# Kernel optimization log

Measured on AMD Instinct MI355X. Metric: run time of the kernel, lower is better.

The kernel has to match this reference:

```python
import jax, jax.numpy as jnp
import numpy as np

B, H, S, DK, DV = 2, 16, 2048, 64, 64


def setup_inputs() -> dict:
    key = jax.random.key(0)
    kq, kk, kv = jax.random.split(key, 3)
    queries = jax.random.normal(kq, (B, H, S, DK), dtype=jnp.float32)
    keys = jax.random.normal(kk, (B, H, S, DK), dtype=jnp.float32)
    values = jax.random.normal(kv, (B, H, S, DV), dtype=jnp.float32)
    # causal boolean mask, broadcastable over batch and heads
    mask = jnp.tril(jnp.ones((S, S), dtype=bool))[None, None, :, :]
    return {"queries": queries, "keys": keys, "values": values, "d_k": DK, "mask": mask}


def reference(queries, keys, values, d_k, mask):
    scale = 1.0 / jnp.sqrt(jnp.float32(d_k))
    # scores: [B, H, S, S]
    scores = jnp.einsum("bhqd,bhkd->bhqk", queries, keys) * scale
    mask_f = mask.astype(jnp.float32)
    scores = scores + (-1e9) * (1.0 - mask_f)
    weights = jax.nn.softmax(scores, axis=-1)
    # second mask step from the original: min(|mask|, |weights|)
    weights = jnp.minimum(jnp.abs(mask_f), jnp.abs(weights))
    return jnp.einsum("bhqk,bhkd->bhqd", weights, values)
```

## Files before the change

kernel.cpp:

```cpp
#include <hip/hip_runtime.h>
#include <hip/hip_bf16.h>

#define B_ 2
#define H_ 16
#define S_ 2048
#define D_ 64

typedef __attribute__((ext_vector_type(8))) short bf16x8;
typedef __attribute__((ext_vector_type(8))) unsigned short u16x8;
typedef __attribute__((ext_vector_type(4))) unsigned int u32x4;
typedef __attribute__((ext_vector_type(4))) float f32x4;
typedef unsigned short ushort_t;

#define SCALE 0.18033688011112042f

__device__ __forceinline__ unsigned short f2bf(float x) {
  unsigned int u = __builtin_bit_cast(unsigned int, x);
  unsigned int r = (u + 0x7FFFu + ((u >> 16) & 1u)) >> 16;
  return (unsigned short)r;
}

__device__ __forceinline__ unsigned int cvt_pk_bf16(float lo, float hi) {
  unsigned int r;
  asm("v_cvt_pk_bf16_f32 %0, %1, %2" : "=v"(r) : "v"(lo), "v"(hi));
  return r;
}

__device__ __forceinline__ float fast_exp2(float x) {
  float r;
  asm("v_exp_f32 %0, %1" : "=v"(r) : "v"(x));
  return r;
}

__device__ __forceinline__ float fmax3(float a, float b, float c) {
  return fmaxf(fmaxf(a, b), c);
}

__device__ __forceinline__ int sigma32(int lr) {
  return (lr & 3) | ((lr & 0x0C) << 1) | ((lr & 0x10) >> 2);
}

#define GLL16(gp, lp)                                                          \
  __builtin_amdgcn_global_load_lds(                                            \
      (const __attribute__((address_space(1))) unsigned int*)(gp),             \
      (__attribute__((address_space(3))) unsigned int*)(lp), 16, 0, 0)

__global__ void prepack32(const float* __restrict__ Kf, const float* __restrict__ Vf,
                          ushort_t* __restrict__ Kg, ushort_t* __restrict__ Vtg) {
  const int blk = blockIdx.x;
  const int tid = threadIdx.x;
  const int bh = blk >> 6, kt = blk & 63;
  const float* srcK = Kf + ((size_t)bh * S_ + (size_t)kt * 32) * D_;
  const float* srcV = Vf + ((size_t)bh * S_ + (size_t)kt * 32) * D_;
  ushort_t* dK = Kg + (size_t)blk * 2048;
  ushort_t* dV = Vtg + (size_t)blk * 2048;
  const int e = tid * 8;
  {
    const int lr = e >> 6, pos = (e >> 3) & 7, ch = pos ^ (lr & 7);
    const float* sp = srcK + sigma32(lr) * 64 + ch * 8;
    float4 a = *(const float4*)sp;
    float4 b = *(const float4*)(sp + 4);
    u16x8 w;
    w[0] = f2bf(a.x); w[1] = f2bf(a.y); w[2] = f2bf(a.z); w[3] = f2bf(a.w);
    w[4] = f2bf(b.x); w[5] = f2bf(b.y); w[6] = f2bf(b.z); w[7] = f2bf(b.w);
    *(u16x8*)(dK + e) = w;
  }
  {
    const int d0 = e >> 5, pos2 = (e >> 3) & 3, ch2 = pos2 ^ (d0 & 3);
    u16x8 w;
    for (int i = 0; i < 8; ++i) w[i] = f2bf(srcV[(size_t)(ch2 * 8 + i) * 64 + d0]);
    *(u16x8*)(dV + e) = w;
  }
}

__launch_bounds__(256, 8)
__global__ void attn_s32(const float* __restrict__ Qf, const ushort_t* __restrict__ Kg,
                         const ushort_t* __restrict__ Vtg, float* __restrict__ O,
                         float* __restrict__ PO, float* __restrict__ ML) {
  const int bh = blockIdx.x;
  const int y = blockIdx.y;
  int qt, c;
  if (y == 0) { qt = 15; c = 0; }
  else if (y <= 16) { qt = 15 + y; c = 0; }
  else if (y == 17) { qt = 31; c = 1; }
  else { const int p = y - 18, k = 15 - (p >> 1);
         if (p & 1) { qt = k + 15; c = 1; } else { qt = k - 1; c = 0; } }
  const int t0k = c << 5;
  const int tEnd = 2 * qt + 1;
  const int t1k = (tEnd < t0k + 31) ? tEnd : (t0k + 31);

  const int tid = threadIdx.x;
  const int wave = tid >> 6, lane = tid & 63;
  const int col = lane & 15, g = lane >> 4;

  __shared__ __align__(16) ushort_t Kl[2][32][64];
  __shared__ __align__(16) ushort_t Vt[2][64][32];

  const int qrow = qt * 64 + wave * 16 + col;
  bf16x8 qf[2];
  {
    const float* Qh = Qf + (size_t)bh * S_ * D_;
    for (int kk = 0; kk < 2; ++kk) {
      const float* p = Qh + (size_t)qrow * 64 + kk * 32 + g * 8;
      float4 a = *(const float4*)p;
      float4 b = *(const float4*)(p + 4);
      float v[8] = {a.x, a.y, a.z, a.w, b.x, b.y, b.z, b.w};
      bf16x8 w;
      for (int i = 0; i < 8; ++i) w[i] = (short)f2bf(v[i] * SCALE);
      qf[kk] = w;
    }
  }

  f32x4 acc[4] = {};
  float m_ = -INFINITY, l_ = 0.0f;

  const int ch0 = (g ^ (col & 7)) << 3;
  const int ch1 = ((4 | g) ^ (col & 7)) << 3;
  const int chV = (g ^ (col & 3)) << 3;

  auto STAGE = [&](int kt, int b) {
    const ushort_t* kg = Kg + ((size_t)(bh * 64 + kt)) * 2048;
    const ushort_t* vg = Vtg + ((size_t)(bh * 64 + kt)) * 2048;
    GLL16(kg + tid * 8, &Kl[b][0][0] + tid * 8);
    GLL16(vg + tid * 8, &Vt[b][0][0] + tid * 8);
  };

  auto COMPUTE = [&](int kt, int b, bool diag) {
    f32x4 s[2] = {{0,0,0,0},{0,0,0,0}};
    __builtin_amdgcn_s_setprio(1);
    #pragma unroll
    for (int nt = 0; nt < 2; ++nt) {
      const ushort_t* row = &Kl[b][nt * 16 + col][0];
      const bf16x8 kf0 = *(const bf16x8*)(row + ch0);
      const bf16x8 kf1 = *(const bf16x8*)(row + ch1);
      s[nt] = __builtin_amdgcn_mfma_f32_16x16x32_bf16(kf0, qf[0], s[nt], 0, 0, 0);
      s[nt] = __builtin_amdgcn_mfma_f32_16x16x32_bf16(kf1, qf[1], s[nt], 0, 0, 0);
    }
    __builtin_amdgcn_s_setprio(0);
    if (diag) {
      const int qg = qt * 64 + wave * 16 + col - 32 * kt - 8 * g;
      #pragma unroll
      for (int nt = 0; nt < 2; ++nt)
        #pragma unroll
        for (int r = 0; r < 4; ++r)
          if (4 * nt + r > qg) s[nt][r] = -INFINITY;
    }
    float pm = fmax3(fmax3(s[0][0], s[0][1], s[0][2]),
                     fmax3(s[0][3], s[1][0], s[1][1]),
                     fmaxf(fmaxf(s[1][2], s[1][3]), -INFINITY));
    pm = fmaxf(pm, __shfl_xor(pm, 16));
    pm = fmaxf(pm, __shfl_xor(pm, 32));
    float fac = 1.0f;
    if (!__all(pm - m_ <= 8.0f)) {
      const float mn = fmaxf(m_, pm);
      fac = fast_exp2(m_ - mn);
      m_ = mn;
      #pragma unroll
      for (int nt = 0; nt < 4; ++nt) acc[nt] *= fac;
    }
    #pragma unroll
    for (int nt = 0; nt < 2; ++nt)
      #pragma unroll
      for (int r = 0; r < 4; ++r) s[nt][r] = fast_exp2(s[nt][r] - m_);
    const float b0 = (s[0][0] + s[0][1]) + (s[0][2] + s[0][3]);
    const float b1 = (s[1][0] + s[1][1]) + (s[1][2] + s[1][3]);
    l_ = l_ * fac + (b0 + b1);
    u32x4 w;
    w[0] = cvt_pk_bf16(s[0][0], s[0][1]); w[1] = cvt_pk_bf16(s[0][2], s[0][3]);
    w[2] = cvt_pk_bf16(s[1][0], s[1][1]); w[3] = cvt_pk_bf16(s[1][2], s[1][3]);
    const bf16x8 pf = __builtin_bit_cast(bf16x8, w);
    __builtin_amdgcn_s_setprio(1);
    #pragma unroll
    for (int nt = 0; nt < 4; ++nt) {
      const bf16x8 vf = *(const bf16x8*)(&Vt[b][nt * 16 + col][0] + chV);
      acc[nt] = __builtin_amdgcn_mfma_f32_16x16x32_bf16(vf, pf, acc[nt], 0, 0, 0);
    }
    __builtin_amdgcn_s_setprio(0);
  };

  int cur = 0;
  STAGE(t0k, 0);
  __syncthreads();
  const int diag0 = 2 * qt;
  for (int kt = t0k; kt <= t1k; ++kt) {
    if (kt < t1k) STAGE(kt + 1, cur ^ 1);
    COMPUTE(kt, cur, kt >= diag0);
    __syncthreads();
    cur ^= 1;
  }

  float lsum = l_;
  lsum += __shfl_xor(lsum, 16);
  lsum += __shfl_xor(lsum, 32);
  const int rowloc = wave * 16 + col;
  if (qt <= 15) {
    const float inv = 1.0f / lsum;
    float* dst = O + (size_t)bh * S_ * D_ + (size_t)qrow * 64;
    #pragma unroll
    for (int nt = 0; nt < 4; ++nt) {
      f32x4 v = acc[nt];
      v *= inv;
      *(f32x4*)(dst + nt * 16 + 4 * g) = v;
    }
  } else {
    float* po = PO + (size_t)((((bh << 4) + (qt - 16)) << 1) + c) * 4096;
    #pragma unroll
    for (int nt = 0; nt < 4; ++nt)
      *(f32x4*)(po + rowloc * 64 + nt * 16 + 4 * g) = acc[nt];
    if (g == 0) {
      float* ml = ML + (size_t)((((bh << 4) + (qt - 16)) << 1) + c) * 128 + rowloc * 2;
      ml[0] = m_;
      ml[1] = lsum;
    }
  }
}

__global__ void merge_partials(const float* __restrict__ PO, const float* __restrict__ ML,
                               float* __restrict__ O) {
  const int bh = blockIdx.x;
  const int q16 = blockIdx.y;
  const int tid = threadIdx.x;
  const int r = tid >> 2, d0 = (tid & 3) << 4;
  const size_t base = (size_t)((bh << 4) + q16) << 1;
  const float* ml0 = ML + base * 128 + r * 2;
  const float* ml1 = ML + (base + 1) * 128 + r * 2;
  const float m0 = ml0[0], l0 = ml0[1], m1 = ml1[0], l1 = ml1[1];
  const float M = fmaxf(m0, m1);
  const float w0 = fast_exp2(m0 - M), w1 = fast_exp2(m1 - M);
  const float inv = 1.0f / (w0 * l0 + w1 * l1);
  const float a = w0 * inv, b = w1 * inv;
  const float* p0 = PO + base * 4096 + r * 64 + d0;
  const float* p1 = PO + (base + 1) * 4096 + r * 64 + d0;
  float* out = O + ((size_t)bh * S_ + (size_t)(16 + q16) * 64 + r) * 64 + d0;
  #pragma unroll
  for (int j = 0; j < 4; ++j) {
    float4 x = *(const float4*)(p0 + 4 * j);
    float4 y = *(const float4*)(p1 + 4 * j);
    float4 o;
    o.x = a * x.x + b * y.x; o.y = a * x.y + b * y.y;
    o.z = a * x.z + b * y.z; o.w = a * x.w + b * y.w;
    *(float4*)(out + 4 * j) = o;
  }
}

__device__ __forceinline__ int sigma_row64(int rl) {
  return (rl & 0x23) | ((rl & 0x0C) << 1) | ((rl & 0x10) >> 2);
}
__launch_bounds__(256, 4)
__global__ void attn_fb(const float* __restrict__ Qf, const float* __restrict__ Kf,
                        const float* __restrict__ Vf, float* __restrict__ O) {
  const int bh = blockIdx.x;
  const int qt = 31 - blockIdx.y;
  const int tid = threadIdx.x;
  const int wave = tid >> 6, lane = tid & 63;
  const int col = lane & 15, g = lane >> 4;
  __shared__ __align__(16) ushort_t Kl[2][64][64];
  __shared__ __align__(16) ushort_t Vt[2][64][64];
  const int qrow = qt * 64 + wave * 16 + col;
  bf16x8 qf[2];
  {
    const float* Qh = Qf + (size_t)bh * S_ * D_;
    for (int kk = 0; kk < 2; ++kk) {
      const float* p = Qh + (size_t)qrow * 64 + kk * 32 + g * 8;
      float4 a = *(const float4*)p;
      float4 b = *(const float4*)(p + 4);
      float v[8] = {a.x, a.y, a.z, a.w, b.x, b.y, b.z, b.w};
      bf16x8 w;
      for (int i = 0; i < 8; ++i) w[i] = (short)f2bf(v[i] * SCALE);
      qf[kk] = w;
    }
  }
  f32x4 acc[4] = {};
  float m_ = -INFINITY, l_ = 0.0f;
  const int ch0 = (g ^ (col & 7)) << 3;
  const int ch1 = ((4 | g) ^ (col & 7)) << 3;
  auto STAGE = [&](int t, int b) {
    const float* Kh = Kf + (size_t)bh * S_ * D_;
    const float* Vh = Vf + (size_t)bh * S_ * D_;
    {
      const int rl = tid >> 2;
      const int c0 = (tid & 3) << 4;
      const float* src = Kh + ((size_t)(t * 64 + sigma_row64(rl))) * 64 + c0;
      for (int jj = 0; jj < 2; ++jj) {
        float4 x = *(const float4*)(src + jj * 8);
        float4 y = *(const float4*)(src + jj * 8 + 4);
        u16x8 w;
        w[0] = f2bf(x.x); w[1] = f2bf(x.y); w[2] = f2bf(x.z); w[3] = f2bf(x.w);
        w[4] = f2bf(y.x); w[5] = f2bf(y.y); w[6] = f2bf(y.z); w[7] = f2bf(y.w);
        const int ch = (c0 >> 3) + jj;
        *(u16x8*)&Kl[b][rl][(ch ^ (rl & 7)) << 3] = w;
      }
    }
    {
      const int cc = tid & 63;
      const int r0 = (tid >> 6) << 4;
      const float* src = Vh + ((size_t)(t * 64 + r0)) * 64 + cc;
      for (int jj = 0; jj < 2; ++jj) {
        u16x8 w;
        for (int i = 0; i < 8; ++i) w[i] = f2bf(src[(size_t)(jj * 8 + i) * 64]);
        const int ch = (r0 >> 3) + jj;
        *(u16x8*)&Vt[b][cc][(ch ^ (cc & 7)) << 3] = w;
      }
    }
  };
  auto COMPUTE = [&](int b, bool diag) {
    f32x4 s[4] = {{0,0,0,0},{0,0,0,0},{0,0,0,0},{0,0,0,0}};
    for (int nt = 0; nt < 4; ++nt) {
      const ushort_t* row = &Kl[b][nt * 16 + col][0];
      const bf16x8 kf0 = *(const bf16x8*)(row + ch0);
      const bf16x8 kf1 = *(const bf16x8*)(row + ch1);
      s[nt] = __builtin_amdgcn_mfma_f32_16x16x32_bf16(kf0, qf[0], s[nt], 0, 0, 0);
      s[nt] = __builtin_amdgcn_mfma_f32_16x16x32_bf16(kf1, qf[1], s[nt], 0, 0, 0);
    }
    if (diag) {
      const int qloc = wave * 16 + col;
      for (int nt = 0; nt < 4; ++nt) {
        const int tb = 32 * (nt >> 1) + 4 * (nt & 1) + 8 * g;
        for (int r = 0; r < 4; ++r)
          if (tb + r > qloc) s[nt][r] = -INFINITY;
      }
    }
    float pm = -INFINITY;
    for (int nt = 0; nt < 4; ++nt)
      for (int r = 0; r < 4; ++r) pm = fmaxf(pm, s[nt][r]);
    pm = fmaxf(pm, __shfl_xor(pm, 16));
    pm = fmaxf(pm, __shfl_xor(pm, 32));
    float fac = 1.0f;
    if (!__all(pm - m_ <= 8.0f)) {
      const float mn = fmaxf(m_, pm);
      fac = fast_exp2(m_ - mn);
      m_ = mn;
      for (int nt = 0; nt < 4; ++nt) acc[nt] *= fac;
    }
    float sum = 0.0f;
    for (int nt = 0; nt < 4; ++nt)
      for (int r = 0; r < 4; ++r) {
        const float p = fast_exp2(s[nt][r] - m_);
        s[nt][r] = p;
        sum += p;
      }
    l_ = l_ * fac + sum;
    u32x4 t0, t1;
    t0[0] = cvt_pk_bf16(s[0][0], s[0][1]); t0[1] = cvt_pk_bf16(s[0][2], s[0][3]);
    t0[2] = cvt_pk_bf16(s[1][0], s[1][1]); t0[3] = cvt_pk_bf16(s[1][2], s[1][3]);
    t1[0] = cvt_pk_bf16(s[2][0], s[2][1]); t1[1] = cvt_pk_bf16(s[2][2], s[2][3]);
    t1[2] = cvt_pk_bf16(s[3][0], s[3][1]); t1[3] = cvt_pk_bf16(s[3][2], s[3][3]);
    const bf16x8 pf0 = __builtin_bit_cast(bf16x8, t0);
    const bf16x8 pf1 = __builtin_bit_cast(bf16x8, t1);
    for (int nt = 0; nt < 4; ++nt) {
      const ushort_t* row = &Vt[b][nt * 16 + col][0];
      const bf16x8 vf0 = *(const bf16x8*)(row + ch0);
      const bf16x8 vf1 = *(const bf16x8*)(row + ch1);
      acc[nt] = __builtin_amdgcn_mfma_f32_16x16x32_bf16(vf0, pf0, acc[nt], 0, 0, 0);
      acc[nt] = __builtin_amdgcn_mfma_f32_16x16x32_bf16(vf1, pf1, acc[nt], 0, 0, 0);
    }
  };
  int cur = 0;
  STAGE(0, 0);
  __syncthreads();
  for (int t = 0; t <= qt; ++t) {
    if (t < qt) STAGE(t + 1, cur ^ 1);
    COMPUTE(cur, t == qt);
    __syncthreads();
    cur ^= 1;
  }
  float lsum = l_;
  lsum += __shfl_xor(lsum, 16);
  lsum += __shfl_xor(lsum, 32);
  const float inv = 1.0f / lsum;
  float* dst = O + (size_t)bh * S_ * D_ + (size_t)qrow * 64;
  for (int nt = 0; nt < 4; ++nt) {
    f32x4 v = acc[nt];
    v *= inv;
    *(f32x4*)(dst + nt * 16 + 4 * g) = v;
  }
}

extern "C" void kernel_launch(void* const* d_in, const int* in_sizes, int n_in,
                              void* d_out, int out_size, void* d_ws, size_t ws_size,
                              hipStream_t stream) {
  const float* Q = (const float*)d_in[0];
  const float* K = (const float*)d_in[1];
  const float* V = (const float*)d_in[2];
  float* O = (float*)d_out;
  const size_t NE = (size_t)B_ * H_ * S_ * D_;
  const size_t needK = 2 * NE * sizeof(ushort_t);
  const size_t PO_elems = 32ull * 16 * 2 * 4096;
  const size_t ML_elems = 32ull * 16 * 2 * 128;
  const size_t needSplit = needK + (PO_elems + ML_elems) * sizeof(float);
  if (ws_size >= needSplit) {
    ushort_t* kg = (ushort_t*)d_ws;
    float* PO = (float*)((char*)d_ws + needK);
    float* ML = PO + PO_elems;
    prepack32<<<2048, 256, 0, stream>>>(K, V, kg, kg + NE);
    attn_s32<<<dim3(32, 48), 256, 0, stream>>>(Q, kg, kg + NE, O, PO, ML);
    merge_partials<<<dim3(32, 16), 256, 0, stream>>>(PO, ML, O);
  } else {
    attn_fb<<<dim3(32, 32), 256, 0, stream>>>(Q, K, V, O);
  }
}
```

Before: 54.83 us.

## Switch attention kernel to 32x32 MFMA with 64-key tiles and intra-block key split

The main attention kernel moves from 16x16x32 MFMA over 32-key tiles to 32x32x16 MFMA over 64-key tiles. Each pair of waves shares a 32-query block and splits each key tile in half, and the two partial softmax states are merged through LDS at the end. The prepack kernel now emits 64-row swizzled K and transposed V tiles, and the running max starts at a finite value. The aim is fewer loop iterations and barriers and better MFMA efficiency, at the cost of double the LDS per block, lower occupancy (launch bounds 4), and an extra cross-wave merge step.

```diff
diff --git a/kernel.cpp b/kernel.cpp
--- a/kernel.cpp
+++ b/kernel.cpp
@@ -9,6 +9,7 @@
 typedef __attribute__((ext_vector_type(8))) short bf16x8;
 typedef __attribute__((ext_vector_type(8))) unsigned short u16x8;
 typedef __attribute__((ext_vector_type(4))) unsigned int u32x4;
+typedef __attribute__((ext_vector_type(16))) float f32x16;
 typedef __attribute__((ext_vector_type(4))) float f32x4;
 typedef unsigned short ushort_t;
 
@@ -35,9 +36,24 @@
 __device__ __forceinline__ float fmax3(float a, float b, float c) {
   return fmaxf(fmaxf(a, b), c);
 }
-
-__device__ __forceinline__ int sigma32(int lr) {
-  return (lr & 3) | ((lr & 0x0C) << 1) | ((lr & 0x10) >> 2);
+__device__ __forceinline__ float vmax16(f32x16 v) {
+  float a = fmax3(v[0], v[1], v[2]);
+  float b = fmax3(v[3], v[4], v[5]);
+  float c = fmax3(v[6], v[7], v[8]);
+  float d = fmax3(v[9], v[10], v[11]);
+  float e = fmax3(v[12], v[13], v[14]);
+  return fmax3(fmax3(a, b, v[15]), fmax3(c, d, e), -INFINITY);
+}
+__device__ __forceinline__ float vsum16(f32x16 v) {
+  float a = (v[0] + v[1]) + (v[2] + v[3]);
+  float b = (v[4] + v[5]) + (v[6] + v[7]);
+  float c = (v[8] + v[9]) + (v[10] + v[11]);
+  float d = (v[12] + v[13]) + (v[14] + v[15]);
+  return (a + b) + (c + d);
+}
+
+__device__ __forceinline__ int sigma6(int rl) {
+  return (rl & 0x33) | ((rl & 4) << 1) | ((rl & 8) >> 1);
 }
 
 #define GLL16(gp, lp)                                                          \
@@ -45,110 +61,109 @@
       (const __attribute__((address_space(1))) unsigned int*)(gp),             \
       (__attribute__((address_space(3))) unsigned int*)(lp), 16, 0, 0)
 
-__global__ void prepack32(const float* __restrict__ Kf, const float* __restrict__ Vf,
-                          ushort_t* __restrict__ Kg, ushort_t* __restrict__ Vtg) {
+__global__ void prepack(const float* __restrict__ Kf, const float* __restrict__ Vf,
+                        ushort_t* __restrict__ Kg, ushort_t* __restrict__ Vtg) {
   const int blk = blockIdx.x;
   const int tid = threadIdx.x;
-  const int bh = blk >> 6, kt = blk & 63;
-  const float* srcK = Kf + ((size_t)bh * S_ + (size_t)kt * 32) * D_;
-  const float* srcV = Vf + ((size_t)bh * S_ + (size_t)kt * 32) * D_;
-  ushort_t* dK = Kg + (size_t)blk * 2048;
-  ushort_t* dV = Vtg + (size_t)blk * 2048;
-  const int e = tid * 8;
-  {
-    const int lr = e >> 6, pos = (e >> 3) & 7, ch = pos ^ (lr & 7);
-    const float* sp = srcK + sigma32(lr) * 64 + ch * 8;
-    float4 a = *(const float4*)sp;
-    float4 b = *(const float4*)(sp + 4);
-    u16x8 w;
-    w[0] = f2bf(a.x); w[1] = f2bf(a.y); w[2] = f2bf(a.z); w[3] = f2bf(a.w);
-    w[4] = f2bf(b.x); w[5] = f2bf(b.y); w[6] = f2bf(b.z); w[7] = f2bf(b.w);
-    *(u16x8*)(dK + e) = w;
-  }
-  {
-    const int d0 = e >> 5, pos2 = (e >> 3) & 3, ch2 = pos2 ^ (d0 & 3);
-    u16x8 w;
-    for (int i = 0; i < 8; ++i) w[i] = f2bf(srcV[(size_t)(ch2 * 8 + i) * 64 + d0]);
-    *(u16x8*)(dV + e) = w;
-  }
-}
-
-__launch_bounds__(256, 8)
-__global__ void attn_s32(const float* __restrict__ Qf, const ushort_t* __restrict__ Kg,
-                         const ushort_t* __restrict__ Vtg, float* __restrict__ O,
-                         float* __restrict__ PO, float* __restrict__ ML) {
+  const int bh = blk >> 5, j = blk & 31;
+  const float* srcK = Kf + ((size_t)bh * S_ + (size_t)j * 64) * D_;
+  const float* srcV = Vf + ((size_t)bh * S_ + (size_t)j * 64) * D_;
+  ushort_t* dK = Kg + (size_t)blk * 4096;
+  ushort_t* dV = Vtg + (size_t)blk * 4096;
+  for (int is = 0; is < 2; ++is) {
+    const int e = is * 2048 + tid * 8;
+    {
+      const int rl = e >> 6, pos = (e >> 3) & 7, ch = pos ^ (rl & 7);
+      const float* sp = srcK + sigma6(rl) * 64 + ch * 8;
+      float4 a = *(const float4*)sp;
+      float4 b = *(const float4*)(sp + 4);
+      u16x8 w;
+      w[0] = f2bf(a.x); w[1] = f2bf(a.y); w[2] = f2bf(a.z); w[3] = f2bf(a.w);
+      w[4] = f2bf(b.x); w[5] = f2bf(b.y); w[6] = f2bf(b.z); w[7] = f2bf(b.w);
+      *(u16x8*)(dK + e) = w;
+    }
+    {
+      const int d0 = e >> 6, pos = (e >> 3) & 7, ch = pos ^ (d0 & 7);
+      u16x8 w;
+      for (int i = 0; i < 8; ++i) w[i] = f2bf(srcV[(size_t)(ch * 8 + i) * 64 + d0]);
+      *(u16x8*)(dV + e) = w;
+    }
+  }
+}
+
+__launch_bounds__(256, 4)
+__global__ void attn_pp(const float* __restrict__ Qf, const ushort_t* __restrict__ Kg,
+                        const ushort_t* __restrict__ Vtg, float* __restrict__ O,
+                        float* __restrict__ PO, float* __restrict__ ML) {
   const int bh = blockIdx.x;
   const int y = blockIdx.y;
   int qt, c;
   if (y == 0) { qt = 15; c = 0; }
   else if (y <= 16) { qt = 15 + y; c = 0; }
   else if (y == 17) { qt = 31; c = 1; }
-  else { const int p = y - 18, k = 15 - (p >> 1);
-         if (p & 1) { qt = k + 15; c = 1; } else { qt = k - 1; c = 0; } }
-  const int t0k = c << 5;
-  const int tEnd = 2 * qt + 1;
-  const int t1k = (tEnd < t0k + 31) ? tEnd : (t0k + 31);
+  else { const int px = y - 18, k = 15 - (px >> 1);
+         if (px & 1) { qt = k + 15; c = 1; } else { qt = k - 1; c = 0; } }
+  const int j0 = c << 4;
+  const int j1 = (qt < j0 + 15) ? qt : (j0 + 15);
 
   const int tid = threadIdx.x;
   const int wave = tid >> 6, lane = tid & 63;
-  const int col = lane & 15, g = lane >> 4;
-
-  __shared__ __align__(16) ushort_t Kl[2][32][64];
-  __shared__ __align__(16) ushort_t Vt[2][64][32];
-
-  const int qrow = qt * 64 + wave * 16 + col;
-  bf16x8 qf[2];
+  const int qh = wave >> 1, p = wave & 1;
+  const int cq = lane & 31, hi = lane >> 5;
+
+  __shared__ __align__(16) ushort_t Kl[2][64][64];
+  __shared__ __align__(16) ushort_t Vt[2][64][64];
+  __shared__ float mlS[2][2][32][2];
+
+  const int qrow = qt * 64 + qh * 32 + cq;
+  bf16x8 qf[4];
   {
-    const float* Qh = Qf + (size_t)bh * S_ * D_;
-    for (int kk = 0; kk < 2; ++kk) {
-      const float* p = Qh + (size_t)qrow * 64 + kk * 32 + g * 8;
-      float4 a = *(const float4*)p;
-      float4 b = *(const float4*)(p + 4);
-      float v[8] = {a.x, a.y, a.z, a.w, b.x, b.y, b.z, b.w};
+    const float* qp = Qf + (size_t)bh * S_ * D_ + (size_t)qrow * D_ + 8 * hi;
+    #pragma unroll
+    for (int ks = 0; ks < 4; ++ks) {
+      float4 a = *(const float4*)(qp + ks * 16);
+      float4 b = *(const float4*)(qp + ks * 16 + 4);
       bf16x8 w;
-      for (int i = 0; i < 8; ++i) w[i] = (short)f2bf(v[i] * SCALE);
-      qf[kk] = w;
-    }
-  }
-
-  f32x4 acc[4] = {};
-  float m_ = -INFINITY, l_ = 0.0f;
-
-  const int ch0 = (g ^ (col & 7)) << 3;
-  const int ch1 = ((4 | g) ^ (col & 7)) << 3;
-  const int chV = (g ^ (col & 3)) << 3;
-
-  auto STAGE = [&](int kt, int b) {
-    const ushort_t* kg = Kg + ((size_t)(bh * 64 + kt)) * 2048;
-    const ushort_t* vg = Vtg + ((size_t)(bh * 64 + kt)) * 2048;
-    GLL16(kg + tid * 8, &Kl[b][0][0] + tid * 8);
-    GLL16(vg + tid * 8, &Vt[b][0][0] + tid * 8);
+      w[0] = (short)f2bf(a.x * SCALE); w[1] = (short)f2bf(a.y * SCALE);
+      w[2] = (short)f2bf(a.z * SCALE); w[3] = (short)f2bf(a.w * SCALE);
+      w[4] = (short)f2bf(b.x * SCALE); w[5] = (short)f2bf(b.y * SCALE);
+      w[6] = (short)f2bf(b.z * SCALE); w[7] = (short)f2bf(b.w * SCALE);
+      qf[ks] = w;
+    }
+  }
+
+  f32x16 acc0 = {}, acc1 = {};
+  float m_ = -30000.0f, l_ = 0.0f;
+  const int xk = cq & 7;
+
+  auto STAGE = [&](int j, int b) {
+    const ushort_t* kg = Kg + ((size_t)(bh * 32 + j)) * 4096;
+    const ushort_t* vg = Vtg + ((size_t)(bh * 32 + j)) * 4096;
+    GLL16(kg + tid * 8,        &Kl[b][0][0] + tid * 8);
+    GLL16(kg + 2048 + tid * 8, &Kl[b][0][0] + 2048 + tid * 8);
+    GLL16(vg + tid * 8,        &Vt[b][0][0] + tid * 8);
+    GLL16(vg + 2048 + tid * 8, &Vt[b][0][0] + 2048 + tid * 8);
   };
 
-  auto COMPUTE = [&](int kt, int b, bool diag) {
-    f32x4 s[2] = {{0,0,0,0},{0,0,0,0}};
+  auto COMPUTE = [&](int b, bool diag) {
+    f32x16 s = {};
+    const ushort_t* krow = &Kl[b][32 * p + cq][0];
     __builtin_amdgcn_s_setprio(1);
     #pragma unroll
-    for (int nt = 0; nt < 2; ++nt) {
-      const ushort_t* row = &Kl[b][nt * 16 + col][0];
-      const bf16x8 kf0 = *(const bf16x8*)(row + ch0);
-      const bf16x8 kf1 = *(const bf16x8*)(row + ch1);
-      s[nt] = __builtin_amdgcn_mfma_f32_16x16x32_bf16(kf0, qf[0], s[nt], 0, 0, 0);
-      s[nt] = __builtin_amdgcn_mfma_f32_16x16x32_bf16(kf1, qf[1], s[nt], 0, 0, 0);
+    for (int ks = 0; ks < 4; ++ks) {
+      const bf16x8 kf = *(const bf16x8*)(krow + (((2 * ks + hi) ^ xk) << 3));
+      s = __builtin_amdgcn_mfma_f32_32x32x16_bf16(kf, qf[ks], s, 0, 0, 0);
     }
     __builtin_amdgcn_s_setprio(0);
     if (diag) {
-      const int qg = qt * 64 + wave * 16 + col - 32 * kt - 8 * g;
+      const int lim = 32 * qh + cq - 32 * p;
       #pragma unroll
-      for (int nt = 0; nt < 2; ++nt)
-        #pragma unroll
-        for (int r = 0; r < 4; ++r)
-          if (4 * nt + r > qg) s[nt][r] = -INFINITY;
-    }
-    float pm = fmax3(fmax3(s[0][0], s[0][1], s[0][2]),
-                     fmax3(s[0][3], s[1][0], s[1][1]),
-                     fmaxf(fmaxf(s[1][2], s[1][3]), -INFINITY));
-    pm = fmaxf(pm, __shfl_xor(pm, 16));
+      for (int r = 0; r < 16; ++r) {
+        const int tau = 16 * (r >> 3) + 4 * ((r >> 2) & 1) + (r & 3) + 8 * hi;
+        if (tau > lim) s[r] = -INFINITY;
+      }
+    }
+    float pm = vmax16(s);
     pm = fmaxf(pm, __shfl_xor(pm, 32));
     float fac = 1.0f;
     if (!__all(pm - m_ <= 8.0f)) {
@@ -156,61 +171,103 @@
       fac = fast_exp2(m_ - mn);
       m_ = mn;
       #pragma unroll
-      for (int nt = 0; nt < 4; ++nt) acc[nt] *= fac;
+      for (int r = 0; r < 16; ++r) { acc0[r] *= fac; acc1[r] *= fac; }
     }
     #pragma unroll
-    for (int nt = 0; nt < 2; ++nt)
-      #pragma unroll
-      for (int r = 0; r < 4; ++r) s[nt][r] = fast_exp2(s[nt][r] - m_);
-    const float b0 = (s[0][0] + s[0][1]) + (s[0][2] + s[0][3]);
-    const float b1 = (s[1][0] + s[1][1]) + (s[1][2] + s[1][3]);
-    l_ = l_ * fac + (b0 + b1);
-    u32x4 w;
-    w[0] = cvt_pk_bf16(s[0][0], s[0][1]); w[1] = cvt_pk_bf16(s[0][2], s[0][3]);
-    w[2] = cvt_pk_bf16(s[1][0], s[1][1]); w[3] = cvt_pk_bf16(s[1][2], s[1][3]);
-    const bf16x8 pf = __builtin_bit_cast(bf16x8, w);
+    for (int r = 0; r < 16; ++r) s[r] = fast_exp2(s[r] - m_);
+    l_ = l_ * fac + vsum16(s);
+    u32x4 t0, t1;
+    t0[0] = cvt_pk_bf16(s[0], s[1]);   t0[1] = cvt_pk_bf16(s[2], s[3]);
+    t0[2] = cvt_pk_bf16(s[4], s[5]);   t0[3] = cvt_pk_bf16(s[6], s[7]);
+    t1[0] = cvt_pk_bf16(s[8], s[9]);   t1[1] = cvt_pk_bf16(s[10], s[11]);
+    t1[2] = cvt_pk_bf16(s[12], s[13]); t1[3] = cvt_pk_bf16(s[14], s[15]);
+    const bf16x8 pf0 = __builtin_bit_cast(bf16x8, t0);
+    const bf16x8 pf1 = __builtin_bit_cast(bf16x8, t1);
+    const ushort_t* v0 = &Vt[b][cq][0];
+    const ushort_t* v1 = &Vt[b][32 + cq][0];
     __builtin_amdgcn_s_setprio(1);
-    #pragma unroll
-    for (int nt = 0; nt < 4; ++nt) {
-      const bf16x8 vf = *(const bf16x8*)(&Vt[b][nt * 16 + col][0] + chV);
-      acc[nt] = __builtin_amdgcn_mfma_f32_16x16x32_bf16(vf, pf, acc[nt], 0, 0, 0);
+    {
+      const bf16x8 a00 = *(const bf16x8*)(v0 + (((4 * p + hi) ^ xk) << 3));
+      const bf16x8 a01 = *(const bf16x8*)(v0 + (((4 * p + 2 + hi) ^ xk) << 3));
+      const bf16x8 a10 = *(const bf16x8*)(v1 + (((4 * p + hi) ^ xk) << 3));
+      const bf16x8 a11 = *(const bf16x8*)(v1 + (((4 * p + 2 + hi) ^ xk) << 3));
+      acc0 = __builtin_amdgcn_mfma_f32_32x32x16_bf16(a00, pf0, acc0, 0, 0, 0);
+      acc0 = __builtin_amdgcn_mfma_f32_32x32x16_bf16(a01, pf1, acc0, 0, 0, 0);
+      acc1 = __builtin_amdgcn_mfma_f32_32x32x16_bf16(a10, pf0, acc1, 0, 0, 0);
+      acc1 = __builtin_amdgcn_mfma_f32_32x32x16_bf16(a11, pf1, acc1, 0, 0, 0);
     }
     __builtin_amdgcn_s_setprio(0);
   };
 
   int cur = 0;
-  STAGE(t0k, 0);
+  STAGE(j0, 0);
   __syncthreads();
-  const int diag0 = 2 * qt;
-  for (int kt = t0k; kt <= t1k; ++kt) {
-    if (kt < t1k) STAGE(kt + 1, cur ^ 1);
-    COMPUTE(kt, cur, kt >= diag0);
+  for (int j = j0; j <= j1; ++j) {
+    if (j < j1) STAGE(j + 1, cur ^ 1);
+    COMPUTE(cur, j == qt);
     __syncthreads();
     cur ^= 1;
   }
 
-  float lsum = l_;
-  lsum += __shfl_xor(lsum, 16);
-  lsum += __shfl_xor(lsum, 32);
-  const int rowloc = wave * 16 + col;
-  if (qt <= 15) {
-    const float inv = 1.0f / lsum;
-    float* dst = O + (size_t)bh * S_ * D_ + (size_t)qrow * 64;
+  float l2 = l_ + __shfl_xor(l_, 32);
+  float* accS0 = (float*)&Kl[0][0][0];
+  float* accS1 = (float*)&Vt[0][0][0];
+  const int sbase = ((qh * 2 + hi) * 32 + cq) * 17;
+  if (p == 1) {
     #pragma unroll
-    for (int nt = 0; nt < 4; ++nt) {
-      f32x4 v = acc[nt];
-      v *= inv;
-      *(f32x4*)(dst + nt * 16 + 4 * g) = v;
-    }
-  } else {
-    float* po = PO + (size_t)((((bh << 4) + (qt - 16)) << 1) + c) * 4096;
-    #pragma unroll
-    for (int nt = 0; nt < 4; ++nt)
-      *(f32x4*)(po + rowloc * 64 + nt * 16 + 4 * g) = acc[nt];
-    if (g == 0) {
-      float* ml = ML + (size_t)((((bh << 4) + (qt - 16)) << 1) + c) * 128 + rowloc * 2;
-      ml[0] = m_;
-      ml[1] = lsum;
+    for (int q2 = 0; q2 < 4; ++q2) {
+      f32x4 w0, w1;
+      #pragma unroll
+      for (int e = 0; e < 4; ++e) { w0[e] = acc0[4 * q2 + e]; w1[e] = acc1[4 * q2 + e]; }
+      *(f32x4*)(accS0 + sbase + 4 * q2) = w0;
+      *(f32x4*)(accS1 + sbase + 4 * q2) = w1;
+    }
+    mlS[qh][hi][cq][0] = m_;
+    mlS[qh][hi][cq][1] = l2;
+  }
+  __syncthreads();
+  if (p == 0) {
+    const float m1 = mlS[qh][hi][cq][0], l1 = mlS[qh][hi][cq][1];
+    const float M = fmaxf(m_, m1);
+    const float w0 = fast_exp2(m_ - M), w1 = fast_exp2(m1 - M);
+    const float L = w0 * l2 + w1 * l1;
+    const int qloc = qh * 32 + cq;
+    if (qt <= 15) {
+      const float inv = 1.0f / L;
+      float* dst = O + (size_t)bh * S_ * D_ + (size_t)qrow * D_;
+      #pragma unroll
+      for (int dt = 0; dt < 2; ++dt)
+        #pragma unroll
+        for (int q2 = 0; q2 < 4; ++q2) {
+          const float* ps = (dt ? accS1 : accS0) + sbase + 4 * q2;
+          f32x4 v;
+          #pragma unroll
+          for (int e = 0; e < 4; ++e) {
+            const float mine = (dt ? acc1[4 * q2 + e] : acc0[4 * q2 + e]);
+            v[e] = (w0 * mine + w1 * ps[e]) * inv;
+          }
+          *(f32x4*)(dst + 32 * dt + 8 * q2 + 4 * hi) = v;
+        }
+    } else {
+      float* po = PO + (size_t)((((bh << 4) + (qt - 16)) << 1) + c) * 4096;
+      #pragma unroll
+      for (int dt = 0; dt < 2; ++dt)
+        #pragma unroll
+        for (int q2 = 0; q2 < 4; ++q2) {
+          const float* ps = (dt ? accS1 : accS0) + sbase + 4 * q2;
+          f32x4 v;
+          #pragma unroll
+          for (int e = 0; e < 4; ++e) {
+            const float mine = (dt ? acc1[4 * q2 + e] : acc0[4 * q2 + e]);
+            v[e] = w0 * mine + w1 * ps[e];
+          }
+          *(f32x4*)(po + qloc * 64 + 32 * dt + 8 * q2 + 4 * hi) = v;
+        }
+      if (hi == 0) {
+        float* ml = ML + (size_t)((((bh << 4) + (qt - 16)) << 1) + c) * 128 + qloc * 2;
+        ml[0] = M;
+        ml[1] = L;
+      }
     }
   }
 }
@@ -243,9 +300,6 @@
   }
 }
 
-__device__ __forceinline__ int sigma_row64(int rl) {
-  return (rl & 0x23) | ((rl & 0x0C) << 1) | ((rl & 0x10) >> 2);
-}
 __launch_bounds__(256, 4)
 __global__ void attn_fb(const float* __restrict__ Qf, const float* __restrict__ Kf,
                         const float* __restrict__ Vf, float* __restrict__ O) {
@@ -261,9 +315,9 @@
   {
     const float* Qh = Qf + (size_t)bh * S_ * D_;
     for (int kk = 0; kk < 2; ++kk) {
-      const float* p = Qh + (size_t)qrow * 64 + kk * 32 + g * 8;
-      float4 a = *(const float4*)p;
-      float4 b = *(const float4*)(p + 4);
+      const float* pp = Qh + (size_t)qrow * 64 + kk * 32 + g * 8;
+      float4 a = *(const float4*)pp;
+      float4 b = *(const float4*)(pp + 4);
       float v[8] = {a.x, a.y, a.z, a.w, b.x, b.y, b.z, b.w};
       bf16x8 w;
       for (int i = 0; i < 8; ++i) w[i] = (short)f2bf(v[i] * SCALE);
@@ -271,7 +325,7 @@
     }
   }
   f32x4 acc[4] = {};
-  float m_ = -INFINITY, l_ = 0.0f;
+  float m_ = -30000.0f, l_ = 0.0f;
   const int ch0 = (g ^ (col & 7)) << 3;
   const int ch1 = ((4 | g) ^ (col & 7)) << 3;
   auto STAGE = [&](int t, int b) {
@@ -280,13 +334,13 @@
     {
       const int rl = tid >> 2;
       const int c0 = (tid & 3) << 4;
-      const float* src = Kh + ((size_t)(t * 64 + sigma_row64(rl))) * 64 + c0;
+      const float* src = Kh + ((size_t)(t * 64 + sigma6(rl))) * 64 + c0;
       for (int jj = 0; jj < 2; ++jj) {
         float4 x = *(const float4*)(src + jj * 8);
-        float4 y = *(const float4*)(src + jj * 8 + 4);
+        float4 yv = *(const float4*)(src + jj * 8 + 4);
         u16x8 w;
         w[0] = f2bf(x.x); w[1] = f2bf(x.y); w[2] = f2bf(x.z); w[3] = f2bf(x.w);
-        w[4] = f2bf(y.x); w[5] = f2bf(y.y); w[6] = f2bf(y.z); w[7] = f2bf(y.w);
+        w[4] = f2bf(yv.x); w[5] = f2bf(yv.y); w[6] = f2bf(yv.z); w[7] = f2bf(yv.w);
         const int ch = (c0 >> 3) + jj;
         *(u16x8*)&Kl[b][rl][(ch ^ (rl & 7)) << 3] = w;
       }
@@ -335,9 +389,9 @@
     float sum = 0.0f;
     for (int nt = 0; nt < 4; ++nt)
       for (int r = 0; r < 4; ++r) {
-        const float p = fast_exp2(s[nt][r] - m_);
-        s[nt][r] = p;
-        sum += p;
+        const float pv = fast_exp2(s[nt][r] - m_);
+        s[nt][r] = pv;
+        sum += pv;
       }
     l_ = l_ * fac + sum;
     u32x4 t0, t1;
@@ -392,8 +446,8 @@
     ushort_t* kg = (ushort_t*)d_ws;
     float* PO = (float*)((char*)d_ws + needK);
     float* ML = PO + PO_elems;
-    prepack32<<<2048, 256, 0, stream>>>(K, V, kg, kg + NE);
-    attn_s32<<<dim3(32, 48), 256, 0, stream>>>(Q, kg, kg + NE, O, PO, ML);
+    prepack<<<1024, 256, 0, stream>>>(K, V, kg, kg + NE);
+    attn_pp<<<dim3(32, 48), 256, 0, stream>>>(Q, kg, kg + NE, O, PO, ML);
     merge_partials<<<dim3(32, 16), 256, 0, stream>>>(PO, ML, O);
   } else {
     attn_fb<<<dim3(32, 32), 256, 0, stream>>>(Q, K, V, O);
```

Result: slower. 57.99 us (+5.8%).
